# Kernel optimization log

Hardware: AMD Instinct MI355X
Metric: run time of the kernel (lower is better)

## Reference

```python
import jax, jax.numpy as jnp
import numpy as np

B, L, D = 32, 512, 1024          # batch, seq_len, bert_dim
M, T, S = 8, 2, 4                # answer lists, texts, disjoint spans per text
NEG = -1e7                       # replace_masked_values fill used by the module


def setup_inputs() -> dict:
    key = jax.random.key(0)
    ks = jax.random.split(key, 8)
    return {
        "bert_out": jax.random.normal(ks[0], (B, L, D), jnp.float32),
        "seq_mask": jnp.ones((B, L), jnp.int32),
        "wordpiece_mask": jnp.ones((B, L), jnp.int32),
        "answer_as_text_to_disjoint_bios": jax.random.randint(ks[1], (B, T, S, L), 0, 3),
        "answer_as_list_of_bios": jax.random.randint(ks[2], (B, M, L), 0, 3),
        "span_bio_labels": jax.random.randint(ks[3], (B, L), 0, 3),
        "is_bio_mask": jnp.ones((B,), jnp.int32),
        # predictor = Linear(D, D) -> ReLU -> (Dropout, eval) -> Linear(D, 3)
        "W1": jax.random.normal(ks[4], (D, D), jnp.float32) / np.sqrt(D),
        "b1": jnp.zeros((D,), jnp.float32),
        "W2": jax.random.normal(ks[5], (D, 3), jnp.float32) / np.sqrt(D),
        "b2": jnp.zeros((3,), jnp.float32),
    }


def reference(bert_out, seq_mask, wordpiece_mask, answer_as_text_to_disjoint_bios,
              answer_as_list_of_bios, span_bio_labels, is_bio_mask,
              W1, b1, W2, b2):
    # ---- module(): FF predictor + masked log-softmax ----
    h = jax.nn.relu(jnp.einsum("bld,dh->blh", bert_out, W1) + b1)
    logits = jnp.einsum("blh,hc->blc", h, W2) + b2            # (B, L, 3)
    log_probs = jax.nn.log_softmax(logits, axis=-1)
    log_probs = log_probs * seq_mask[:, :, None].astype(log_probs.dtype)  # masked -> 0.0

    # ---- log_likelihood(), generation_top_k == 0 branch ----
    ab = answer_as_list_of_bios * seq_mask[:, None, :]        # (B, M, L)
    is_pregen = (ab.sum((1, 2)) > 0).astype(jnp.int32)        # (B,)
    extra = (span_bio_labels * (1 - is_pregen)[:, None])[:, None, :]  # (B, 1, L)
    list_of_bios = jnp.concatenate([ab, extra], axis=1)       # (B, M+1, L)

    # ---- _get_combined_likelihood: gather tag log-probs per candidate sequence ----
    ll = jnp.take_along_axis(log_probs[:, None], list_of_bios[..., None], axis=-1)[..., 0]  # (B, M+1, L)
    pad = list_of_bios.sum(-1) > 0                             # (B, M+1) non-empty sequences
    ll = ll * pad[..., None]
    seq_ll = jnp.where(pad, ll.sum(-1), NEG)                   # (B, M+1)
    lml = jax.nn.logsumexp(seq_ll, axis=-1)                    # (B,)
    return jnp.where(is_bio_mask.astype(bool), lml, NEG)
```

## Files before the change

### kernel.cpp

```cpp
#include <hip/hip_runtime.h>
#include <hip/hip_bf16.h>
#include <cstdint>

#define GLOBAL_AS __attribute__((address_space(1)))
#define LDS_AS    __attribute__((address_space(3)))

typedef float f4v  __attribute__((ext_vector_type(4)));

#define NEGV (-1e7f)

__device__ __forceinline__ void gload_lds16(const void* g, void* l) {
  __builtin_amdgcn_global_load_lds((const GLOBAL_AS uint32_t*)g,
                                   (LDS_AS uint32_t*)l, 16, 0, 0);
}

__device__ __forceinline__ unsigned char f2fp8(float x) {
  return (unsigned char)(__builtin_amdgcn_cvt_pk_fp8_f32(x, x, 0, false) & 0xff);
}

__global__ __launch_bounds__(256) void cvt_all(const float* __restrict__ bert,
                                               unsigned char* __restrict__ afp8,
                                               const float* __restrict__ w1,
                                               unsigned char* __restrict__ w1t) {
  __shared__ float tile[32][33];
  if (blockIdx.x < 2048) {
    const int n8 = 16384 * 1024 / 8;
    int i = blockIdx.x * 256 + threadIdx.x;
    for (; i < n8; i += 2048 * 256) {
      float4 a = ((const float4*)bert)[2 * i + 0];
      float4 b = ((const float4*)bert)[2 * i + 1];
      int lo = __builtin_amdgcn_cvt_pk_fp8_f32(a.x * 16.f, a.y * 16.f, 0, false);
      lo     = __builtin_amdgcn_cvt_pk_fp8_f32(a.z * 16.f, a.w * 16.f, lo, true);
      int hi = __builtin_amdgcn_cvt_pk_fp8_f32(b.x * 16.f, b.y * 16.f, 0, false);
      hi     = __builtin_amdgcn_cvt_pk_fp8_f32(b.z * 16.f, b.w * 16.f, hi, true);
      ((int2*)afp8)[i] = make_int2(lo, hi);
    }
  } else {
    int bb = blockIdx.x - 2048;
    int bx = bb & 31;
    int by = bb >> 5;
    int tx = threadIdx.x & 31;
    int ty = threadIdx.x >> 5;
#pragma unroll
    for (int j = 0; j < 4; ++j) {
      int kk = ty + j * 8;
      tile[kk][tx] = w1[(size_t)(by * 32 + kk) * 1024 + bx * 32 + tx];
    }
    __syncthreads();
#pragma unroll
    for (int j = 0; j < 4; ++j) {
      int nn = ty + j * 8;
      w1t[(size_t)(bx * 32 + nn) * 1024 + by * 32 + tx] = f2fp8(tile[tx][nn] * 128.f);
    }
  }
}

__global__ __launch_bounds__(256, 2) void gemm_fused(
    const unsigned char* __restrict__ Afp8,
    const unsigned char* __restrict__ Bfp8,
    const float* __restrict__ b1,
    const float* __restrict__ W2,
    float* __restrict__ partials)
{
  __shared__ __align__(16) char lds[65536];

  int bid = blockIdx.x;
  int wid = (bid & 7) * 128 + (bid >> 3);
  int mt = wid >> 3;
  int nt = wid & 7;

  int tid  = threadIdx.x;
  int lane = tid & 63;
  int wv   = tid >> 6;
  int wr   = wv >> 1;
  int wc   = wv & 1;

  int laneq = lane & 15;
  int klo8  = (lane >> 4) * 8;
  int sw    = (laneq & 7) << 4;

  const size_t arow0 = (size_t)mt * 128;
  const size_t brow0 = (size_t)nt * 128;

  int scol = ((lane & 7) * 16) ^ ((lane >> 3) << 4);
  const unsigned char* gA = Afp8 + (arow0 + wv * 32 + (lane >> 3)) * 1024 + scol;
  const unsigned char* gB = Bfp8 + (brow0 + wv * 32 + (lane >> 3)) * 1024 + scol;

  f4v acc[4][4];
#pragma unroll
  for (int m = 0; m < 4; ++m)
#pragma unroll
    for (int n = 0; n < 4; ++n)
      acc[m][n] = f4v{0.f, 0.f, 0.f, 0.f};

  auto STAGE = [&](int t) {
    char* base = lds + ((t & 1) << 15);
#pragma unroll
    for (int c = 0; c < 4; ++c) {
      gload_lds16(gA + (size_t)(c * 8) * 1024 + t * 128, base + (wv * 4 + c) * 1024);
      gload_lds16(gB + (size_t)(c * 8) * 1024 + t * 128, base + 16384 + (wv * 4 + c) * 1024);
    }
  };

  auto COMPUTE = [&](int buf) {
    const char* As = lds + (buf << 15);
    const char* Bs = As + 16384;
    long av[4][4], bv[4][4];
#pragma unroll
    for (int m = 0; m < 4; ++m) {
      int ra = wr * 64 + m * 16 + laneq;
      const char* p = As + ra * 128;
#pragma unroll
      for (int kh = 0; kh < 4; ++kh)
        av[m][kh] = *(const long*)(p + ((kh * 32 + klo8) ^ sw));
    }
#pragma unroll
    for (int n = 0; n < 4; ++n) {
      int rb = wc * 64 + n * 16 + laneq;
      const char* p = Bs + rb * 128;
#pragma unroll
      for (int kh = 0; kh < 4; ++kh)
        bv[n][kh] = *(const long*)(p + ((kh * 32 + klo8) ^ sw));
    }
    __builtin_amdgcn_s_setprio(1);
#pragma unroll
    for (int m = 0; m < 4; ++m)
#pragma unroll
      for (int n = 0; n < 4; ++n)
#pragma unroll
        for (int kh = 0; kh < 4; ++kh)
          acc[m][n] = __builtin_amdgcn_mfma_f32_16x16x32_fp8_fp8(
              av[m][kh], bv[n][kh], acc[m][n], 0, 0, 0);
    __builtin_amdgcn_s_setprio(0);
  };

  STAGE(0);
  asm volatile("s_waitcnt vmcnt(0)" ::: "memory");
  __builtin_amdgcn_s_barrier();

  for (int t = 0; t < 8; ++t) {
    if (t < 7) {
      STAGE(t + 1);
      asm volatile("s_waitcnt vmcnt(8)" ::: "memory");
    } else {
      asm volatile("s_waitcnt vmcnt(0)" ::: "memory");
    }
    __builtin_amdgcn_s_barrier();
    __builtin_amdgcn_sched_barrier(0);
    COMPUTE(t & 1);
    __builtin_amdgcn_s_barrier();
  }

  const float DS = 1.0f / 2048.0f;
  float b1v[4];
  float w2v[4][3];
#pragma unroll
  for (int n = 0; n < 4; ++n) {
    int gc = nt * 128 + wc * 64 + n * 16 + laneq;
    b1v[n] = b1[gc];
    w2v[n][0] = W2[gc * 3 + 0];
    w2v[n][1] = W2[gc * 3 + 1];
    w2v[n][2] = W2[gc * 3 + 2];
  }
  float* red = (float*)lds;
#pragma unroll
  for (int m = 0; m < 4; ++m) {
#pragma unroll
    for (int q = 0; q < 4; ++q) {
      float p0 = 0.f, p1 = 0.f, p2 = 0.f;
#pragma unroll
      for (int n = 0; n < 4; ++n) {
        float h = acc[m][n][q] * DS + b1v[n];
        h = fmaxf(h, 0.f);
        p0 += h * w2v[n][0];
        p1 += h * w2v[n][1];
        p2 += h * w2v[n][2];
      }
#pragma unroll
      for (int s = 1; s < 16; s <<= 1) {
        p0 += __shfl_xor(p0, s, 64);
        p1 += __shfl_xor(p1, s, 64);
        p2 += __shfl_xor(p2, s, 64);
      }
      if ((lane & 15) == 0) {
        int row = wr * 64 + m * 16 + (lane >> 4) * 4 + q;
        red[(wc * 128 + row) * 3 + 0] = p0;
        red[(wc * 128 + row) * 3 + 1] = p1;
        red[(wc * 128 + row) * 3 + 2] = p2;
      }
    }
  }
  __syncthreads();
  if (tid < 128) {
    float s0 = 0.f, s1 = 0.f, s2 = 0.f;
#pragma unroll
    for (int w = 0; w < 2; ++w) {
      s0 += red[(w * 128 + tid) * 3 + 0];
      s1 += red[(w * 128 + tid) * 3 + 1];
      s2 += red[(w * 128 + tid) * 3 + 2];
    }
    size_t o = ((size_t)nt * 16384 + (size_t)mt * 128 + tid) * 3;
    partials[o + 0] = s0;
    partials[o + 1] = s1;
    partials[o + 2] = s2;
  }
}

__device__ __forceinline__ float blockReduceSum(float v, float* red, int t) {
#pragma unroll
  for (int s = 32; s >= 1; s >>= 1) v += __shfl_xor(v, s, 64);
  __syncthreads();
  if ((t & 63) == 0) red[t >> 6] = v;
  __syncthreads();
  return red[0] + red[1] + red[2] + red[3];
}

__global__ __launch_bounds__(256) void finalize(
    const float* __restrict__ partials,
    const float* __restrict__ b2,
    const int* __restrict__ seq_mask,
    const int* __restrict__ ans,
    const int* __restrict__ span,
    const int* __restrict__ isbio,
    float* __restrict__ out)
{
  int b = blockIdx.x;
  int t = threadIdx.x;
  __shared__ float lp[512][3];
  __shared__ float red[4];
  __shared__ float seq_ll[9];
  __shared__ int preg;

  float b20 = b2[0], b21 = b2[1], b22 = b2[2];
  const int NP = 16384 * 3;

  for (int l = t; l < 512; l += 256) {
    int gi = b * 512 + l;
    float x0 = b20, x1 = b21, x2 = b22;
#pragma unroll
    for (int w = 0; w < 8; ++w) {
      x0 += partials[w * NP + gi * 3 + 0];
      x1 += partials[w * NP + gi * 3 + 1];
      x2 += partials[w * NP + gi * 3 + 2];
    }
    float mx = fmaxf(x0, fmaxf(x1, x2));
    float lse = mx + logf(expf(x0 - mx) + expf(x1 - mx) + expf(x2 - mx));
    float msk = (float)seq_mask[gi];
    lp[l][0] = (x0 - lse) * msk;
    lp[l][1] = (x1 - lse) * msk;
    lp[l][2] = (x2 - lse) * msk;
  }
  __syncthreads();

  float s = 0.f;
  for (int i = t; i < 8 * 512; i += 256) {
    int m = i >> 9, l = i & 511;
    s += (float)(ans[(b * 8 + m) * 512 + l] * seq_mask[b * 512 + l]);
  }
  s = blockReduceSum(s, red, t);
  if (t == 0) preg = (s > 0.f) ? 1 : 0;
  __syncthreads();
  int ip = preg;

  for (int m = 0; m < 9; ++m) {
    float sll = 0.f, sidx = 0.f;
    for (int l = t; l < 512; l += 256) {
      int idx;
      if (m < 8) idx = ans[(b * 8 + m) * 512 + l] * seq_mask[b * 512 + l];
      else       idx = span[b * 512 + l] * (1 - ip);
      sll  += lp[l][idx];
      sidx += (float)idx;
    }
    sll  = blockReduceSum(sll, red, t);
    sidx = blockReduceSum(sidx, red, t);
    if (t == 0) seq_ll[m] = (sidx > 0.f) ? sll : NEGV;
  }

  if (t == 0) {
    float mx = seq_ll[0];
#pragma unroll
    for (int m = 1; m < 9; ++m) mx = fmaxf(mx, seq_ll[m]);
    float sum = 0.f;
#pragma unroll
    for (int m = 0; m < 9; ++m) sum += expf(seq_ll[m] - mx);
    float lml = mx + logf(sum);
    out[b] = isbio[b] ? lml : NEGV;
  }
}

extern "C" void kernel_launch(void* const* d_in, const int* in_sizes, int n_in,
                              void* d_out, int out_size, void* d_ws, size_t ws_size,
                              hipStream_t stream) {
  const float* bert     = (const float*)d_in[0];
  const int*   seq_mask = (const int*)d_in[1];
  const int*   ans      = (const int*)d_in[4];
  const int*   span     = (const int*)d_in[5];
  const int*   isbio    = (const int*)d_in[6];
  const float* W1       = (const float*)d_in[7];
  const float* b1       = (const float*)d_in[8];
  const float* W2       = (const float*)d_in[9];
  const float* b2       = (const float*)d_in[10];
  float* out = (float*)d_out;

  char* ws = (char*)d_ws;
  float* partials      = (float*)ws;
  unsigned char* Afp8  = (unsigned char*)(ws + (2u << 20));
  unsigned char* W1T8  = (unsigned char*)(ws + (18u << 20));

  cvt_all<<<3072, 256, 0, stream>>>(bert, Afp8, W1, W1T8);
  gemm_fused<<<1024, 256, 0, stream>>>(Afp8, W1T8, b1, W2, partials);
  finalize<<<32, 256, 0, stream>>>(partials, b2, seq_mask, ans, span, isbio, out);
}
```

Before: 68.01 us.

## Pre-permute fp8 operands in global memory so LDS fragment reads use 16-byte loads

The conversion kernel now writes A and W1^T in a permuted, pre-swizzled k-order within each 128-byte chunk. Each lane's four 8-byte MFMA k-fragments then sit in two contiguous 16-byte runs. The GEMM copies chunks to LDS unswizzled and reads fragments with two 128-bit LDS loads instead of four 64-bit ones. This cuts LDS instruction count in the inner loop, at the cost of scattered 8-byte and single-byte global writes in the conversion kernel.

Result: slower. 70.66 us (+3.9%).

```diff
diff --git a/kernel.cpp b/kernel.cpp
--- a/kernel.cpp
+++ b/kernel.cpp
@@ -6,6 +6,7 @@
 #define LDS_AS    __attribute__((address_space(3)))
 
 typedef float f4v  __attribute__((ext_vector_type(4)));
+typedef long  lv2  __attribute__((ext_vector_type(2)));
 
 #define NEGV (-1e7f)
 
@@ -33,7 +34,13 @@
       lo     = __builtin_amdgcn_cvt_pk_fp8_f32(a.z * 16.f, a.w * 16.f, lo, true);
       int hi = __builtin_amdgcn_cvt_pk_fp8_f32(b.x * 16.f, b.y * 16.f, 0, false);
       hi     = __builtin_amdgcn_cvt_pk_fp8_f32(b.z * 16.f, b.w * 16.f, hi, true);
-      ((int2*)afp8)[i] = make_int2(lo, hi);
+      int r   = i >> 7;
+      int kg  = i & 127;
+      int t   = kg >> 4;
+      int kh_ = (kg >> 2) & 3;
+      int q   = kg & 3;
+      int dest = r * 1024 + t * 128 + (((q << 5) | (kh_ << 3)) ^ ((r & 7) << 4));
+      *(int2*)(afp8 + dest) = make_int2(lo, hi);
     }
   } else {
     int bb = blockIdx.x - 2048;
@@ -47,10 +54,15 @@
       tile[kk][tx] = w1[(size_t)(by * 32 + kk) * 1024 + bx * 32 + tx];
     }
     __syncthreads();
+    int t   = by >> 2;
+    int kh_ = by & 3;
+    int q   = tx >> 3;
+    int b   = tx & 7;
 #pragma unroll
     for (int j = 0; j < 4; ++j) {
-      int nn = ty + j * 8;
-      w1t[(size_t)(bx * 32 + nn) * 1024 + by * 32 + tx] = f2fp8(tile[tx][nn] * 128.f);
+      int nrow = bx * 32 + ty + j * 8;
+      w1t[(size_t)nrow * 1024 + t * 128 +
+          (((q << 5) | (kh_ << 3) | b) ^ ((nrow & 7) << 4))] = f2fp8(tile[tx][ty + j * 8] * 128.f);
     }
   }
 }
@@ -76,13 +88,12 @@
   int wc   = wv & 1;
 
   int laneq = lane & 15;
-  int klo8  = (lane >> 4) * 8;
-  int sw    = (laneq & 7) << 4;
+  int q32   = (lane >> 4) << 5;
 
   const size_t arow0 = (size_t)mt * 128;
   const size_t brow0 = (size_t)nt * 128;
 
-  int scol = ((lane & 7) * 16) ^ ((lane >> 3) << 4);
+  int scol = (lane & 7) * 16;
   const unsigned char* gA = Afp8 + (arow0 + wv * 32 + (lane >> 3)) * 1024 + scol;
   const unsigned char* gB = Bfp8 + (brow0 + wv * 32 + (lane >> 3)) * 1024 + scol;
 
@@ -110,17 +121,19 @@
     for (int m = 0; m < 4; ++m) {
       int ra = wr * 64 + m * 16 + laneq;
       const char* p = As + ra * 128;
-#pragma unroll
-      for (int kh = 0; kh < 4; ++kh)
-        av[m][kh] = *(const long*)(p + ((kh * 32 + klo8) ^ sw));
+      int e4 = (ra & 7) << 4;
+      lv2 r1 = *(const lv2*)(p + (q32 ^ e4));
+      lv2 r2 = *(const lv2*)(p + ((q32 + 16) ^ e4));
+      av[m][0] = r1.x; av[m][1] = r1.y; av[m][2] = r2.x; av[m][3] = r2.y;
     }
 #pragma unroll
     for (int n = 0; n < 4; ++n) {
       int rb = wc * 64 + n * 16 + laneq;
       const char* p = Bs + rb * 128;
-#pragma unroll
-      for (int kh = 0; kh < 4; ++kh)
-        bv[n][kh] = *(const long*)(p + ((kh * 32 + klo8) ^ sw));
+      int e4 = (rb & 7) << 4;
+      lv2 r1 = *(const lv2*)(p + (q32 ^ e4));
+      lv2 r2 = *(const lv2*)(p + ((q32 + 16) ^ e4));
+      bv[n][0] = r1.x; bv[n][1] = r1.y; bv[n][2] = r2.x; bv[n][3] = r2.y;
     }
     __builtin_amdgcn_s_setprio(1);
 #pragma unroll
```
